# Kernel tuning notes

Hardware: AMD Instinct MI355X
Metric: run time of the kernel (lower is better)

Reference implementation:

```python
import math
import jax, jax.numpy as jnp
import numpy as np

N_HEADS = 32
N_KV_HEADS = 8
HEAD_DIM = 128
DIM = 4096
B = 32
MAX_SEQ = 4096
Q_LEN = 1
START_POS = 4095


def setup_inputs() -> dict:
    key = jax.random.key(0)
    ks = jax.random.split(key, 9)
    x = jax.random.normal(ks[0], (B, Q_LEN, DIM), dtype=jnp.float32)
    # RoPE angles for the current positions (seqlen=Q_LEN, half head_dim pairs)
    inv_freq = 1.0 / (500000.0 ** (np.arange(0, HEAD_DIM, 2, dtype=np.float32) / HEAD_DIM))
    pos = np.arange(START_POS, START_POS + Q_LEN, dtype=np.float32)
    ang = pos[:, None] * inv_freq[None, :]  # [Q_LEN, HEAD_DIM//2]
    freqs_cos = jnp.asarray(np.cos(ang), dtype=jnp.float32)
    freqs_sin = jnp.asarray(np.sin(ang), dtype=jnp.float32)
    cache_k = jax.random.normal(ks[1], (B, MAX_SEQ, N_KV_HEADS, HEAD_DIM), dtype=jnp.float32)
    cache_v = jax.random.normal(ks[2], (B, MAX_SEQ, N_KV_HEADS, HEAD_DIM), dtype=jnp.float32)
    s = 0.02
    wq = jax.random.normal(ks[3], (N_HEADS * HEAD_DIM, DIM), dtype=jnp.float32) * s
    wk = jax.random.normal(ks[4], (N_KV_HEADS * HEAD_DIM, DIM), dtype=jnp.float32) * s
    wv = jax.random.normal(ks[5], (N_KV_HEADS * HEAD_DIM, DIM), dtype=jnp.float32) * s
    wo = jax.random.normal(ks[6], (DIM, N_HEADS * HEAD_DIM), dtype=jnp.float32) * s
    return {"x": x, "start_pos": START_POS, "freqs_cos": freqs_cos, "freqs_sin": freqs_sin,
            "cache_k": cache_k, "cache_v": cache_v, "wq": wq, "wk": wk, "wv": wv, "wo": wo}


def _rope(t, cos, sin):
    # t: [B, S, h, hd]; cos/sin: [S, hd//2]; complex multiply on (even, odd) pairs
    tr = t.reshape(*t.shape[:-1], HEAD_DIM // 2, 2)
    a, b = tr[..., 0], tr[..., 1]
    c = cos[None, :, None, :]
    s = sin[None, :, None, :]
    out = jnp.stack([a * c - b * s, a * s + b * c], axis=-1)
    return out.reshape(t.shape)


def reference(x, start_pos, freqs_cos, freqs_sin, cache_k, cache_v, wq, wk, wv, wo):
    bsz, seqlen, _ = x.shape
    n_rep = N_HEADS // N_KV_HEADS
    xq = jnp.einsum('bsd,od->bso', x, wq).reshape(bsz, seqlen, N_HEADS, HEAD_DIM)
    xk = jnp.einsum('bsd,od->bso', x, wk).reshape(bsz, seqlen, N_KV_HEADS, HEAD_DIM)
    xv = jnp.einsum('bsd,od->bso', x, wv).reshape(bsz, seqlen, N_KV_HEADS, HEAD_DIM)
    xq = _rope(xq, freqs_cos, freqs_sin)
    xk = _rope(xk, freqs_cos, freqs_sin)
    # KV-cache update (start_pos is a static Python int)
    cache_k = cache_k.at[:, start_pos:start_pos + seqlen].set(xk)
    cache_v = cache_v.at[:, start_pos:start_pos + seqlen].set(xv)
    keys = cache_k[:, :start_pos + seqlen]    # [B, T, Hkv, hd]
    values = cache_v[:, :start_pos + seqlen]  # [B, T, Hkv, hd]
    # GQA: group query heads [H] -> [Hkv, n_rep]; avoids materializing repeated KV
    q = xq.reshape(bsz, seqlen, N_KV_HEADS, n_rep, HEAD_DIM)
    scale = 1.0 / math.sqrt(HEAD_DIM)
    scores = jnp.einsum('bsgrd,btgd->bgrst', q, keys) * scale  # [B, Hkv, n_rep, S, T]
    probs = jax.nn.softmax(scores, axis=-1)
    out = jnp.einsum('bgrst,btgd->bsgrd', probs, values)
    out = out.reshape(bsz, seqlen, N_HEADS * HEAD_DIM)
    return jnp.einsum('bse,de->bsd', out, wo)
```

## Files before the change

### kernel.cpp

```cpp
#include <hip/hip_runtime.h>

#define B_    32
#define DIM_  4096
#define NH_   32
#define NKV_  8
#define HD_   128
#define TSEQ  4096
#define NQKV  6144
#define GSPLIT 32
#define BK    32
#define NT    256
#define TSPL  8
#define TS    512

typedef float f4_t __attribute__((ext_vector_type(4)));

__device__ __forceinline__ f4_t ntl(const float* p) {
    return __builtin_nontemporal_load((const f4_t*)p);
}

__global__ __launch_bounds__(128) void gemm32(
    const float* __restrict__ A, const float* __restrict__ w0,
    const float* __restrict__ w1, const float* __restrict__ w2,
    int b1, int b2, int N, float* __restrict__ po)
{
    __shared__ __align__(16) float wt[BK][NT + 4];
    __shared__ __align__(16) float xp[128][36];
    const int tid = threadIdx.x;
    const int cg  = tid & 31;
    const int bg  = tid >> 5;
    const int ct  = blockIdx.x * NT;
    const int k0  = blockIdx.y * (DIM_ / GSPLIT);

    const float* wb_; int c0_;
    if (ct < b1)      { wb_ = w0; c0_ = ct; }
    else if (ct < b2) { wb_ = w1; c0_ = ct - b1; }
    else              { wb_ = w2; c0_ = ct - b2; }

    {
        const int kq = (tid & 31) * 4;
        const int rr = tid >> 5;
        #pragma unroll
        for (int st = 0; st < 8; ++st) {
            const int bb = st * 4 + rr;
            const float4 xv = *(const float4*)(A + (size_t)bb * DIM_ + k0 + kq);
            xp[kq + 0][bb] = xv.x; xp[kq + 1][bb] = xv.y;
            xp[kq + 2][bb] = xv.z; xp[kq + 3][bb] = xv.w;
        }
    }

    const int kq2 = (tid & 7) * 4;
    const int rr2 = tid >> 3;
    f4_t wreg[16];

    #pragma unroll
    for (int st = 0; st < 16; ++st)
        wreg[st] = ntl(wb_ + (size_t)(c0_ + st * 16 + rr2) * DIM_ + k0 + kq2);
    #pragma unroll
    for (int st = 0; st < 16; ++st) {
        const int c = st * 16 + rr2;
        wt[kq2 + 0][c] = wreg[st][0]; wt[kq2 + 1][c] = wreg[st][1];
        wt[kq2 + 2][c] = wreg[st][2]; wt[kq2 + 3][c] = wreg[st][3];
    }
    __syncthreads();

    float acc[8][8];
    #pragma unroll
    for (int i = 0; i < 8; ++i)
        #pragma unroll
        for (int j = 0; j < 8; ++j) acc[i][j] = 0.f;

    for (int t = 0; t < 4; ++t) {
        if (t < 3) {
            #pragma unroll
            for (int st = 0; st < 16; ++st)
                wreg[st] = ntl(wb_ + (size_t)(c0_ + st * 16 + rr2) * DIM_
                               + k0 + (t + 1) * BK + kq2);
        }
        #pragma unroll 8
        for (int kk = 0; kk < BK; ++kk) {
            const int kr = t * BK + kk;
            const float4 xa = *(const float4*)&xp[kr][bg * 8];
            const float4 xb = *(const float4*)&xp[kr][bg * 8 + 4];
            const float4 wa = *(const float4*)&wt[kk][cg * 4];
            const float4 wb4 = *(const float4*)&wt[kk][128 + cg * 4];
            const float xv[8] = {xa.x, xa.y, xa.z, xa.w, xb.x, xb.y, xb.z, xb.w};
            const float wv[8] = {wa.x, wa.y, wa.z, wa.w, wb4.x, wb4.y, wb4.z, wb4.w};
            #pragma unroll
            for (int i = 0; i < 8; ++i)
                #pragma unroll
                for (int j = 0; j < 8; ++j)
                    acc[i][j] = fmaf(xv[i], wv[j], acc[i][j]);
        }
        __syncthreads();
        if (t < 3) {
            #pragma unroll
            for (int st = 0; st < 16; ++st) {
                const int c = st * 16 + rr2;
                wt[kq2 + 0][c] = wreg[st][0]; wt[kq2 + 1][c] = wreg[st][1];
                wt[kq2 + 2][c] = wreg[st][2]; wt[kq2 + 3][c] = wreg[st][3];
            }
            __syncthreads();
        }
    }

    const size_t srow = (size_t)blockIdx.y * B_;
    #pragma unroll
    for (int i = 0; i < 8; ++i) {
        const int b = bg * 8 + i;
        const float4 o0 = make_float4(acc[i][0], acc[i][1], acc[i][2], acc[i][3]);
        const float4 o1 = make_float4(acc[i][4], acc[i][5], acc[i][6], acc[i][7]);
        *(float4*)&po[(srow + b) * N + ct + cg * 4]       = o0;
        *(float4*)&po[(srow + b) * N + ct + 128 + cg * 4] = o1;
    }
}

__global__ void reduce_rope(const float* __restrict__ po,
                            const float* __restrict__ fc, const float* __restrict__ fs,
                            float* __restrict__ qkv)
{
    const int pid = blockIdx.x * 256 + threadIdx.x;
    const int b  = pid / (NQKV / 4);
    const int c0 = (pid - b * (NQKV / 4)) * 4;
    f4_t v = {0.f, 0.f, 0.f, 0.f};
    #pragma unroll
    for (int s = 0; s < GSPLIT; ++s)
        v += *(const f4_t*)(po + ((size_t)s * B_ + b) * NQKV + c0);
    if (c0 < DIM_ + NKV_ * HD_) {
        const int i = (c0 & 127) >> 1;
        const float ca = fc[i],     sa = fs[i];
        const float cb = fc[i + 1], sb = fs[i + 1];
        f4_t o;
        o[0] = v[0] * ca - v[1] * sa;
        o[1] = v[0] * sa + v[1] * ca;
        o[2] = v[2] * cb - v[3] * sb;
        o[3] = v[2] * sb + v[3] * cb;
        v = o;
    }
    *(f4_t*)(qkv + (size_t)b * NQKV + c0) = v;
}

__device__ __forceinline__ void attn_step(const f4_t kc, const f4_t vc,
                                          const f4_t* q, f4_t* acc, float* l)
{
    float p0 = kc[0]*q[0][0] + kc[1]*q[0][1] + kc[2]*q[0][2] + kc[3]*q[0][3];
    float p1 = kc[0]*q[1][0] + kc[1]*q[1][1] + kc[2]*q[1][2] + kc[3]*q[1][3];
    float p2 = kc[0]*q[2][0] + kc[1]*q[2][1] + kc[2]*q[2][2] + kc[3]*q[2][3];
    float p3 = kc[0]*q[3][0] + kc[1]*q[3][1] + kc[2]*q[3][2] + kc[3]*q[3][3];
    #pragma unroll
    for (int off = 1; off < 32; off <<= 1) {
        p0 += __shfl_xor(p0, off);
        p1 += __shfl_xor(p1, off);
        p2 += __shfl_xor(p2, off);
        p3 += __shfl_xor(p3, off);
    }
    const float scale = 0.08838834764831845f;
    p0 = __expf(p0 * scale); p1 = __expf(p1 * scale);
    p2 = __expf(p2 * scale); p3 = __expf(p3 * scale);
    l[0] += p0; l[1] += p1; l[2] += p2; l[3] += p3;
    acc[0] += p0 * vc; acc[1] += p1 * vc;
    acc[2] += p2 * vc; acc[3] += p3 * vc;
}

__global__ __launch_bounds__(256) void attn_partial(
    const float* __restrict__ qkv, const float* __restrict__ ck,
    const float* __restrict__ cv,
    float* __restrict__ po , float* __restrict__ pl )
{
    const int blk = blockIdx.x;
    const int s = blk & (TSPL - 1);
    const int g = (blk / TSPL) & 7;
    const int b = blk / (TSPL * NKV_);
    const int tid  = threadIdx.x;
    const int grp  = tid >> 5;
    const int lane = tid & 31;
    const int wv   = tid >> 6;
    const int d4   = lane * 4;
    const float* qb = qkv + (size_t)b * NQKV;

    f4_t q[4];
    #pragma unroll
    for (int h = 0; h < 4; ++h)
        q[h] = *(const f4_t*)(qb + (g * 4 + h) * HD_ + d4);

    f4_t zero4 = {0.f, 0.f, 0.f, 0.f};
    f4_t acc[4] = {zero4, zero4, zero4, zero4};
    float l[4] = {0.f, 0.f, 0.f, 0.f};

    const int t0 = s * TS + grp;
    int niter = TS / 8;
    const bool fresh = (s == TSPL - 1) && (grp == 7);
    if (fresh) --niter;

    const size_t base = (((size_t)b * TSEQ + t0) * NKV_ + g) * HD_ + d4;
    const float* kp = ck + base;
    const float* vp = cv + base;
    const size_t step = (size_t)8 * NKV_ * HD_;

    f4_t kc = ntl(kp), vc = ntl(vp);
    for (int it = 0; it < niter - 1; ++it) {
        kp += step; vp += step;
        const f4_t kn = ntl(kp);
        const f4_t vn = ntl(vp);
        attn_step(kc, vc, q, acc, l);
        kc = kn; vc = vn;
    }
    attn_step(kc, vc, q, acc, l);
    if (fresh) {
        const f4_t kf = *(const f4_t*)(qb + DIM_ + g * HD_ + d4);
        const f4_t vf = *(const f4_t*)(qb + DIM_ + NKV_ * HD_ + g * HD_ + d4);
        attn_step(kf, vf, q, acc, l);
    }

    #pragma unroll
    for (int h = 0; h < 4; ++h) {
        #pragma unroll
        for (int e = 0; e < 4; ++e) acc[h][e] += __shfl_xor(acc[h][e], 32);
        l[h] += __shfl_xor(l[h], 32);
    }

    __shared__ __align__(16) float ob[4][4][HD_];
    __shared__ float lb[4][4];
    if ((tid & 32) == 0) {
        #pragma unroll
        for (int h = 0; h < 4; ++h) *(f4_t*)&ob[wv][h][d4] = acc[h];
        if (lane == 0) {
            lb[wv][0] = l[0]; lb[wv][1] = l[1]; lb[wv][2] = l[2]; lb[wv][3] = l[3];
        }
    }
    __syncthreads();
    #pragma unroll
    for (int e = tid; e < 512; e += 256) {
        const float sum = ob[0][e >> 7][e & 127] + ob[1][e >> 7][e & 127]
                        + ob[2][e >> 7][e & 127] + ob[3][e >> 7][e & 127];
        po[(size_t)blk * 512 + e] = sum;
    }
    if (tid < 4)
        pl[blk * 4 + tid] = lb[0][tid] + lb[1][tid] + lb[2][tid] + lb[3][tid];
}

__global__ void attn_combine(const float* __restrict__ po, const float* __restrict__ pl,
                             float* __restrict__ ao)
{
    const int bg  = blockIdx.x;
    const int tid = threadIdx.x;
    const int e0  = tid * 4;
    const int r   = e0 >> 7;
    f4_t o = {0.f, 0.f, 0.f, 0.f};
    float ls = 0.f;
    #pragma unroll
    for (int s = 0; s < TSPL; ++s) {
        o += *(const f4_t*)&po[((size_t)bg * TSPL + s) * 512 + e0];
        ls += pl[(bg * TSPL + s) * 4 + r];
    }
    o *= (1.f / ls);
    const int b = bg >> 3, g = bg & 7;
    *(f4_t*)&ao[(size_t)b * DIM_ + g * 512 + e0] = o;
}

__global__ void reduce_out(const float* __restrict__ po, float* __restrict__ out)
{
    const int pid = blockIdx.x * 256 + threadIdx.x;
    const int b  = pid >> 10;
    const int c0 = (pid & 1023) * 4;
    f4_t v = {0.f, 0.f, 0.f, 0.f};
    #pragma unroll
    for (int s = 0; s < GSPLIT; ++s)
        v += *(const f4_t*)(po + ((size_t)s * B_ + b) * DIM_ + c0);
    *(f4_t*)(out + (size_t)b * DIM_ + c0) = v;
}

extern "C" void kernel_launch(void* const* d_in, const int* in_sizes, int n_in,
                              void* d_out, int out_size, void* d_ws, size_t ws_size,
                              hipStream_t stream)
{
    (void)in_sizes; (void)n_in; (void)out_size; (void)ws_size;
    const float* x  = (const float*)d_in[0];
    const float* fc = (const float*)d_in[2];
    const float* fs = (const float*)d_in[3];
    const float* ck = (const float*)d_in[4];
    const float* cv = (const float*)d_in[5];
    const float* wq = (const float*)d_in[6];
    const float* wk = (const float*)d_in[7];
    const float* wv = (const float*)d_in[8];
    const float* wo = (const float*)d_in[9];
    float* out = (float*)d_out;
    float* ws  = (float*)d_ws;

    float* qkv  = ws;
    float* aout = ws + 196608;
    float* apo  = ws + 327680;
    float* apl  = ws + 1376256;
    float* gp   = ws + 1384448;

    gemm32<<<dim3(NQKV / NT, GSPLIT), 128, 0, stream>>>(
        x, wq, wk, wv, DIM_, DIM_ + NKV_ * HD_, NQKV, gp);
    reduce_rope<<<dim3(B_ * (NQKV / 4) / 256), 256, 0, stream>>>(gp, fc, fs, qkv);
    attn_partial<<<dim3(B_ * NKV_ * TSPL), 256, 0, stream>>>(qkv, ck, cv, apo, apl);
    attn_combine<<<dim3(B_ * NKV_), 128, 0, stream>>>(apo, apl, aout);
    gemm32<<<dim3(DIM_ / NT, GSPLIT), 128, 0, stream>>>(
        aout, wo, wo, wo, DIM_, DIM_, DIM_, gp);
    reduce_out<<<dim3(B_ * DIM_ / 4 / 256), 256, 0, stream>>>(gp, out);
}
```

Baseline: 268.6 us.

## Remap attention so each block covers all KV heads; widen GEMM blocks

The attention partial kernel now assigns one block per (batch, sequence split) and gives each wavefront-half one KV head, so each block reads contiguous full rows of the KV cache (all 8 heads) over 128 positions. This replaces the per-head strided access and removes the shared-memory cross-warp reduction. The sequence split grows from 8 to 32, which enlarges the partial buffers and the combine work. The GEMM also moves to 256 threads per block with half the per-thread accumulator tile, which lowers register pressure and may raise occupancy, at the cost of less reuse per thread.

```diff
diff --git a/kernel.cpp b/kernel.cpp
--- a/kernel.cpp
+++ b/kernel.cpp
@@ -10,8 +10,8 @@
 #define GSPLIT 32
 #define BK    32
 #define NT    256
-#define TSPL  8
-#define TS    512
+#define TSPL  32
+#define TS    128
 
 typedef float f4_t __attribute__((ext_vector_type(4)));
 
@@ -19,16 +19,16 @@
     return __builtin_nontemporal_load((const f4_t*)p);
 }
 
-__global__ __launch_bounds__(128) void gemm32(
+__global__ __launch_bounds__(256) void gemm32(
     const float* __restrict__ A, const float* __restrict__ w0,
     const float* __restrict__ w1, const float* __restrict__ w2,
     int b1, int b2, int N, float* __restrict__ po)
 {
     __shared__ __align__(16) float wt[BK][NT + 4];
-    __shared__ __align__(16) float xp[128][36];
+    __shared__ __align__(16) float xp[128][33];
     const int tid = threadIdx.x;
-    const int cg  = tid & 31;
-    const int bg  = tid >> 5;
+    const int cg  = tid & 63;
+    const int bg  = tid >> 6;
     const int ct  = blockIdx.x * NT;
     const int k0  = blockIdx.y * (DIM_ / GSPLIT);
 
@@ -41,8 +41,8 @@
         const int kq = (tid & 31) * 4;
         const int rr = tid >> 5;
         #pragma unroll
-        for (int st = 0; st < 8; ++st) {
-            const int bb = st * 4 + rr;
+        for (int st = 0; st < 4; ++st) {
+            const int bb = st * 8 + rr;
             const float4 xv = *(const float4*)(A + (size_t)bb * DIM_ + k0 + kq);
             xp[kq + 0][bb] = xv.x; xp[kq + 1][bb] = xv.y;
             xp[kq + 2][bb] = xv.z; xp[kq + 3][bb] = xv.w;
@@ -51,30 +51,30 @@
 
     const int kq2 = (tid & 7) * 4;
     const int rr2 = tid >> 3;
-    f4_t wreg[16];
-
-    #pragma unroll
-    for (int st = 0; st < 16; ++st)
-        wreg[st] = ntl(wb_ + (size_t)(c0_ + st * 16 + rr2) * DIM_ + k0 + kq2);
-    #pragma unroll
-    for (int st = 0; st < 16; ++st) {
-        const int c = st * 16 + rr2;
+    f4_t wreg[8];
+
+    #pragma unroll
+    for (int st = 0; st < 8; ++st)
+        wreg[st] = ntl(wb_ + (size_t)(c0_ + st * 32 + rr2) * DIM_ + k0 + kq2);
+    #pragma unroll
+    for (int st = 0; st < 8; ++st) {
+        const int c = st * 32 + rr2;
         wt[kq2 + 0][c] = wreg[st][0]; wt[kq2 + 1][c] = wreg[st][1];
         wt[kq2 + 2][c] = wreg[st][2]; wt[kq2 + 3][c] = wreg[st][3];
     }
     __syncthreads();
 
-    float acc[8][8];
+    float acc[8][4];
     #pragma unroll
     for (int i = 0; i < 8; ++i)
         #pragma unroll
-        for (int j = 0; j < 8; ++j) acc[i][j] = 0.f;
+        for (int j = 0; j < 4; ++j) acc[i][j] = 0.f;
 
     for (int t = 0; t < 4; ++t) {
         if (t < 3) {
             #pragma unroll
-            for (int st = 0; st < 16; ++st)
-                wreg[st] = ntl(wb_ + (size_t)(c0_ + st * 16 + rr2) * DIM_
+            for (int st = 0; st < 8; ++st)
+                wreg[st] = ntl(wb_ + (size_t)(c0_ + st * 32 + rr2) * DIM_
                                + k0 + (t + 1) * BK + kq2);
         }
         #pragma unroll 8
@@ -83,20 +83,19 @@
             const float4 xa = *(const float4*)&xp[kr][bg * 8];
             const float4 xb = *(const float4*)&xp[kr][bg * 8 + 4];
             const float4 wa = *(const float4*)&wt[kk][cg * 4];
-            const float4 wb4 = *(const float4*)&wt[kk][128 + cg * 4];
             const float xv[8] = {xa.x, xa.y, xa.z, xa.w, xb.x, xb.y, xb.z, xb.w};
-            const float wv[8] = {wa.x, wa.y, wa.z, wa.w, wb4.x, wb4.y, wb4.z, wb4.w};
+            const float wv[4] = {wa.x, wa.y, wa.z, wa.w};
             #pragma unroll
             for (int i = 0; i < 8; ++i)
                 #pragma unroll
-                for (int j = 0; j < 8; ++j)
+                for (int j = 0; j < 4; ++j)
                     acc[i][j] = fmaf(xv[i], wv[j], acc[i][j]);
         }
         __syncthreads();
         if (t < 3) {
             #pragma unroll
-            for (int st = 0; st < 16; ++st) {
-                const int c = st * 16 + rr2;
+            for (int st = 0; st < 8; ++st) {
+                const int c = st * 32 + rr2;
                 wt[kq2 + 0][c] = wreg[st][0]; wt[kq2 + 1][c] = wreg[st][1];
                 wt[kq2 + 2][c] = wreg[st][2]; wt[kq2 + 3][c] = wreg[st][3];
             }
@@ -108,10 +107,8 @@
     #pragma unroll
     for (int i = 0; i < 8; ++i) {
         const int b = bg * 8 + i;
-        const float4 o0 = make_float4(acc[i][0], acc[i][1], acc[i][2], acc[i][3]);
-        const float4 o1 = make_float4(acc[i][4], acc[i][5], acc[i][6], acc[i][7]);
-        *(float4*)&po[(srow + b) * N + ct + cg * 4]       = o0;
-        *(float4*)&po[(srow + b) * N + ct + 128 + cg * 4] = o1;
+        const float4 o = make_float4(acc[i][0], acc[i][1], acc[i][2], acc[i][3]);
+        *(float4*)&po[(srow + b) * N + ct + cg * 4] = o;
     }
 }
 
@@ -169,12 +166,10 @@
 {
     const int blk = blockIdx.x;
     const int s = blk & (TSPL - 1);
-    const int g = (blk / TSPL) & 7;
-    const int b = blk / (TSPL * NKV_);
+    const int b = blk >> 5;
     const int tid  = threadIdx.x;
-    const int grp  = tid >> 5;
+    const int g    = tid >> 5;
     const int lane = tid & 31;
-    const int wv   = tid >> 6;
     const int d4   = lane * 4;
     const float* qb = qkv + (size_t)b * NQKV;
 
@@ -187,15 +182,14 @@
     f4_t acc[4] = {zero4, zero4, zero4, zero4};
     float l[4] = {0.f, 0.f, 0.f, 0.f};
 
-    const int t0 = s * TS + grp;
-    int niter = TS / 8;
-    const bool fresh = (s == TSPL - 1) && (grp == 7);
-    if (fresh) --niter;
-
-    const size_t base = (((size_t)b * TSEQ + t0) * NKV_ + g) * HD_ + d4;
+    const int t0 = s * TS;
+    const bool last = (s == TSPL - 1);
+    const int niter = TS - (last ? 1 : 0);
+
+    const size_t base = ((size_t)b * TSEQ + t0) * (NKV_ * HD_) + tid * 4;
     const float* kp = ck + base;
     const float* vp = cv + base;
-    const size_t step = (size_t)8 * NKV_ * HD_;
+    const int step = NKV_ * HD_;
 
     f4_t kc = ntl(kp), vc = ntl(vp);
     for (int it = 0; it < niter - 1; ++it) {
@@ -206,37 +200,20 @@
         kc = kn; vc = vn;
     }
     attn_step(kc, vc, q, acc, l);
-    if (fresh) {
-        const f4_t kf = *(const f4_t*)(qb + DIM_ + g * HD_ + d4);
-        const f4_t vf = *(const f4_t*)(qb + DIM_ + NKV_ * HD_ + g * HD_ + d4);
+    if (last) {
+        const f4_t kf = *(const f4_t*)(qb + DIM_ + tid * 4);
+        const f4_t vf = *(const f4_t*)(qb + DIM_ + NKV_ * HD_ + tid * 4);
         attn_step(kf, vf, q, acc, l);
     }
 
-    #pragma unroll
-    for (int h = 0; h < 4; ++h) {
-        #pragma unroll
-        for (int e = 0; e < 4; ++e) acc[h][e] += __shfl_xor(acc[h][e], 32);
-        l[h] += __shfl_xor(l[h], 32);
-    }
-
-    __shared__ __align__(16) float ob[4][4][HD_];
-    __shared__ float lb[4][4];
-    if ((tid & 32) == 0) {
-        #pragma unroll
-        for (int h = 0; h < 4; ++h) *(f4_t*)&ob[wv][h][d4] = acc[h];
-        if (lane == 0) {
-            lb[wv][0] = l[0]; lb[wv][1] = l[1]; lb[wv][2] = l[2]; lb[wv][3] = l[3];
-        }
-    }
-    __syncthreads();
-    #pragma unroll
-    for (int e = tid; e < 512; e += 256) {
-        const float sum = ob[0][e >> 7][e & 127] + ob[1][e >> 7][e & 127]
-                        + ob[2][e >> 7][e & 127] + ob[3][e >> 7][e & 127];
-        po[(size_t)blk * 512 + e] = sum;
-    }
-    if (tid < 4)
-        pl[blk * 4 + tid] = lb[0][tid] + lb[1][tid] + lb[2][tid] + lb[3][tid];
+    float* pob = po + (((size_t)(b * NKV_ + g) * TSPL) + s) * 512;
+    #pragma unroll
+    for (int h = 0; h < 4; ++h)
+        *(f4_t*)&pob[h * HD_ + d4] = acc[h];
+    if (lane == 0) {
+        float* plb = pl + ((size_t)(b * NKV_ + g) * TSPL + s) * 4;
+        plb[0] = l[0]; plb[1] = l[1]; plb[2] = l[2]; plb[3] = l[3];
+    }
 }
 
 __global__ void attn_combine(const float* __restrict__ po, const float* __restrict__ pl,
@@ -248,10 +225,10 @@
     const int r   = e0 >> 7;
     f4_t o = {0.f, 0.f, 0.f, 0.f};
     float ls = 0.f;
-    #pragma unroll
+    #pragma unroll 8
     for (int s = 0; s < TSPL; ++s) {
         o += *(const f4_t*)&po[((size_t)bg * TSPL + s) * 512 + e0];
-        ls += pl[(bg * TSPL + s) * 4 + r];
+        ls += pl[((size_t)bg * TSPL + s) * 4 + r];
     }
     o *= (1.f / ls);
     const int b = bg >> 3, g = bg & 7;
@@ -290,15 +267,15 @@
     float* qkv  = ws;
     float* aout = ws + 196608;
     float* apo  = ws + 327680;
-    float* apl  = ws + 1376256;
-    float* gp   = ws + 1384448;
-
-    gemm32<<<dim3(NQKV / NT, GSPLIT), 128, 0, stream>>>(
+    float* apl  = ws + 4521984;
+    float* gp   = ws + 4554752;
+
+    gemm32<<<dim3(NQKV / NT, GSPLIT), 256, 0, stream>>>(
         x, wq, wk, wv, DIM_, DIM_ + NKV_ * HD_, NQKV, gp);
     reduce_rope<<<dim3(B_ * (NQKV / 4) / 256), 256, 0, stream>>>(gp, fc, fs, qkv);
-    attn_partial<<<dim3(B_ * NKV_ * TSPL), 256, 0, stream>>>(qkv, ck, cv, apo, apl);
+    attn_partial<<<dim3(B_ * TSPL), 256, 0, stream>>>(qkv, ck, cv, apo, apl);
     attn_combine<<<dim3(B_ * NKV_), 128, 0, stream>>>(apo, apl, aout);
-    gemm32<<<dim3(DIM_ / NT, GSPLIT), 128, 0, stream>>>(
+    gemm32<<<dim3(DIM_ / NT, GSPLIT), 256, 0, stream>>>(
         aout, wo, wo, wo, DIM_, DIM_, DIM_, gp);
     reduce_out<<<dim3(B_ * DIM_ / 4 / 256), 256, 0, stream>>>(gp, out);
 }
```

After: 249.4 us. 7.2% less time.
